# Kernel tuning notes

Hardware: AMD Instinct MI355X
Metric: run time of the kernel (lower is better)

The kernel has to match this reference:

```python
import jax, jax.numpy as jnp
import numpy as np

TAPS = 5
DELAY = 3
ITERATIONS = 2
EPS = 1e-10


def _wpe_one_iteration(Y, power):
    # Y: (B, F, C, T) complex64, power: (B, F, T) float32
    B, F, C, T = Y.shape
    inv_p = 1.0 / jnp.clip(power, EPS)
    Tq = T - DELAY - TAPS + 1  # number of valid frames
    # signal_framing(Y, TAPS, 1)[..., :Tq, :] then reverse last dim:
    # Y_tilde[..., t, k] = Y[..., t + TAPS - 1 - k]  -> (B, F, C, Tq, TAPS)
    Y_tilde = jnp.stack(
        [Y[..., TAPS - 1 - k: TAPS - 1 - k + Tq] for k in range(TAPS)], axis=-1)
    Y_tilde_ip = Y_tilde * inv_p[..., None, DELAY + TAPS - 1:, None]
    # correlation matrix (B, F, taps*C, taps*C)
    R = jnp.einsum('bfdtk,bfetl->bfkdle', jnp.conj(Y_tilde_ip), Y_tilde)
    R = R.reshape(B, F, TAPS * C, TAPS * C)
    # correlation vector (B, F, taps, C, C): indices (k, e, d)
    P = jnp.einsum('bfdtk,bfet->bfked', jnp.conj(Y_tilde_ip),
                   Y[..., DELAY + TAPS - 1:])
    # regularize and invert (batched small complex systems)
    R = R + EPS * jnp.eye(TAPS * C, dtype=R.dtype)
    inv_R = jnp.linalg.inv(R)
    # (B,F,k,e,d) -> (B,F,e,k,d) -> (B,F,C,taps*C)
    vec = jnp.transpose(P, (0, 1, 3, 2, 4)).reshape(B, F, C, TAPS * C)
    # stacked = vec @ inv_R^T  -> (B, F, C, taps*C)
    stacked = jnp.einsum('bfck,bflk->bfcl', vec, inv_R)
    # (B,F,C1,taps,C2) -> filter_matrix_conj (B,F,taps,C2,C1)
    G_conj = jnp.transpose(stacked.reshape(B, F, C, TAPS, C), (0, 1, 3, 4, 2))
    # delayed copies of Y: Y_shift[..., p, :, t] = Y[..., t - DELAY - p] (zero-padded)
    Y_shift = jnp.stack(
        [jnp.pad(Y[..., :T - DELAY - p], [(0, 0)] * 3 + [(DELAY + p, 0)])
         for p in range(TAPS)], axis=-3)  # (B, F, taps, C, T)
    reverb_tail = jnp.einsum('bfpde,bfpdt->bfet', G_conj, Y_shift)
    return Y - reverb_tail


def setup_inputs() -> dict:
    key = jax.random.key(0)
    k1, k2, k3 = jax.random.split(key, 3)
    B, T, C, F = 8, 600, 8, 257
    data_real = jax.random.normal(k1, (B, T, C, F), dtype=jnp.float32)
    data_imag = jax.random.normal(k2, (B, T, C, F), dtype=jnp.float32)
    ilens = jax.random.randint(k3, (B,), 300, T + 1)
    return {"data_real": data_real, "data_imag": data_imag, "ilens": ilens}


def reference(data_real, data_imag, ilens):
    # data: (B, T, C, F) -> (B, F, C, T)
    Y = jax.lax.complex(data_real, data_imag)
    Y = jnp.transpose(Y, (0, 3, 2, 1))
    B, F, C, T = Y.shape
    # use_dnn_mask=False: power averaged over channels -> (B, F, T)
    power = (Y.real ** 2 + Y.imag ** 2).mean(axis=-2)
    enhanced = Y
    for i in range(ITERATIONS):
        if i > 0:
            power = (enhanced.real ** 2 + enhanced.imag ** 2).mean(axis=-2)
        enhanced = _wpe_one_iteration(Y, power)
    # zero out padded frames (make_pad_mask along T)
    tmask = (jnp.arange(T) < ilens[:, None]).astype(enhanced.real.dtype)
    enhanced = enhanced * tmask[:, None, None, :]
    # back to (B, T, C, F)
    enhanced = jnp.transpose(enhanced, (0, 3, 2, 1))
    return enhanced.real, enhanced.imag
```

## Files before the change

### kernel.cpp

```cpp
#include <hip/hip_runtime.h>
#include <hip/hip_bf16.h>

#define Bb 8
#define Tt 600
#define Cc 8
#define Ff 257
#define TAPS 5
#define DELAY 3
#define KC 40
#define NC 48
#define RPW 52
#define TQ 593
#define TP 602
#define EPSF 1e-10f
#define NTOT (Bb*Tt*Cc*Ff)

__device__ __forceinline__ float2 cmul2(float2 a, float2 b) {
  return make_float2(a.x*b.x - a.y*b.y, a.x*b.y + a.y*b.x);
}

#define CMAC(acc, ax, ay, b)                    \
  acc.x = fmaf(ax, b.x, acc.x);                 \
  acc.x = fmaf(ay, b.y, acc.x);                 \
  acc.y = fmaf(ax, b.y, acc.y);                 \
  acc.y = fmaf(-(ay), b.x, acc.y);

__global__ __launch_bounds__(256) void k_tin(const float* __restrict__ in_re,
                                             const float* __restrict__ in_im,
                                             float2* __restrict__ Yt) {
  __shared__ float2 tile[32][33];
  int f0 = blockIdx.x * 32, t0 = blockIdx.y * 32;
  int b = blockIdx.z >> 3, c = blockIdx.z & 7;
  int tx = threadIdx.x & 31, ty = threadIdx.x >> 5;
#pragma unroll
  for (int ii = 0; ii < 4; ++ii) {
    int t = t0 + ty + 8 * ii, f = f0 + tx;
    if (t < Tt && f < Ff) {
      size_t idx = (((size_t)b * Tt + t) * Cc + c) * Ff + f;
      tile[ty + 8 * ii][tx] = make_float2(in_re[idx], in_im[idx]);
    }
  }
  __syncthreads();
#pragma unroll
  for (int ii = 0; ii < 4; ++ii) {
    int f = f0 + ty + 8 * ii, t = t0 + tx;
    if (f < Ff && t < Tt) {
      size_t o = (((size_t)b * Ff + f) * Cc + c) * Tt + t;
      Yt[o] = tile[tx][ty + 8 * ii];
    }
  }
}

#define ABODY(u) do {                                                     \
  float2 ynd = Yd[tb + (u) + 4];                                          \
  float2 yne = Ye[tb + (u) + 4];                                          \
  float2 yep = Ye[tb + (u) + 7];                                          \
  float w = wl[tb + (u) + 7];                                             \
  wd[((u)+4)%5] = ynd; we[((u)+4)%5] = yne;                               \
  float ax[5], ay[5];                                                     \
  _Pragma("unroll")                                                       \
  for (int k = 0; k < 5; ++k) {                                           \
    float2 yr = wd[((u)+4-k)%5]; ax[k] = w*yr.x; ay[k] = w*yr.y;          \
  }                                                                       \
  _Pragma("unroll")                                                       \
  for (int l = 0; l < 5; ++l) {                                           \
    float2 yc = we[((u)+4-l)%5];                                          \
    _Pragma("unroll")                                                     \
    for (int k = 0; k < 5; ++k) { CMAC(rac[k][l], ax[k], ay[k], yc); }    \
  }                                                                       \
  _Pragma("unroll")                                                       \
  for (int k = 0; k < 5; ++k) { CMAC(pac[k], ax[k], ay[k], yep); }        \
} while (0)

__global__ __launch_bounds__(512, 4) void k_wpe(const float2* __restrict__ Yt,
                                                float2* __restrict__ enh,
                                                const float* __restrict__ in_re,
                                                const float* __restrict__ in_im,
                                                const int* __restrict__ ilens,
                                                float* __restrict__ out_re,
                                                float* __restrict__ out_im,
                                                int load_direct, int store_direct) {
  __shared__ float2 Yl[Cc][TP];
  __shared__ float2 RP[KC][RPW];
  __shared__ float wl[Tt];

  int bf = blockIdx.x;
  int b = bf / Ff, f = bf % Ff;
  int tid = threadIdx.x;
  int group = tid >> 6;
  int lane = tid & 63;
  int d = lane & 7;
  int e = lane >> 3;

  if (!load_direct) {
    const float4* Yg = (const float4*)(Yt + (size_t)bf * (Cc * Tt));
    for (int i = tid; i < Cc * Tt / 2; i += 512) {
      float4 v = Yg[i];
      int c = i / (Tt / 2), t2 = (i % (Tt / 2)) * 2;
      *(float4*)&Yl[c][t2] = v;
    }
  } else {
    for (int i = tid; i < Cc * Tt; i += 512) {
      int c = i / Tt, t = i % Tt;
      size_t idx = (((size_t)b * Tt + t) * Cc + c) * Ff + f;
      Yl[c][t] = make_float2(in_re[idx], in_im[idx]);
    }
  }
  __syncthreads();

  const float2* Yd = &Yl[d][0];
  const float2* Ye = &Yl[e][0];

  int tA = (TQ * group) >> 3;
  int tB = (TQ * (group + 1)) >> 3;

  for (int iter = 0; iter < 3; ++iter) {
    if (iter == 0) {
      for (int t = tid; t < Tt; t += 512) {
        float s = 0.f;
#pragma unroll
        for (int c = 0; c < Cc; ++c) { float2 y = Yl[c][t]; s += y.x*y.x + y.y*y.y; }
        wl[t] = 1.0f / fmaxf(s * 0.125f, EPSF);
      }
    } else {
      for (int t = tid; t < Tt; t += 512) {
        float2 acc[Cc];
#pragma unroll
        for (int ee = 0; ee < Cc; ++ee) acc[ee] = Yl[ee][t];
        for (int p = 0; p < TAPS; ++p) {
          int ts = t - DELAY - p;
          if (ts < 0) break;
#pragma unroll
          for (int dd = 0; dd < Cc; ++dd) {
            float2 u = Yl[dd][ts];
            int j = p * Cc + dd;
#pragma unroll
            for (int ee = 0; ee < Cc; ++ee) {
              float2 g = RP[j][KC + ee];
              acc[ee].x -= g.x*u.x - g.y*u.y;
              acc[ee].y -= g.x*u.y + g.y*u.x;
            }
          }
        }
        if (iter == 1) {
          float s = 0.f;
#pragma unroll
          for (int ee = 0; ee < Cc; ++ee) s += acc[ee].x*acc[ee].x + acc[ee].y*acc[ee].y;
          wl[t] = 1.0f / fmaxf(s * 0.125f, EPSF);
        } else {
          if (!store_direct) {
            float2* Eg = enh + (size_t)bf * (Cc * Tt);
#pragma unroll
            for (int ee = 0; ee < Cc; ++ee) Eg[ee * Tt + t] = acc[ee];
          } else {
            int il = ilens[b];
            bool live = (t < il);
#pragma unroll
            for (int ee = 0; ee < Cc; ++ee) {
              float2 v = live ? acc[ee] : make_float2(0.f, 0.f);
              size_t idx = (((size_t)b * Tt + t) * Cc + ee) * Ff + f;
              out_re[idx] = v.x;
              out_im[idx] = v.y;
            }
          }
        }
      }
    }
    if (iter == 2) break;
    __syncthreads();

    float2 rac[5][5], pac[5];
#pragma unroll
    for (int k = 0; k < 5; ++k) {
#pragma unroll
      for (int l = 0; l < 5; ++l) rac[k][l] = make_float2(0.f, 0.f);
      pac[k] = make_float2(0.f, 0.f);
    }

    float2 wd[5], we[5];
#pragma unroll
    for (int i = 0; i < 4; ++i) { wd[i] = Yd[tA + i]; we[i] = Ye[tA + i]; }

    int tb = tA;
    for (; tb + 5 <= tB; tb += 5) {
      ABODY(0); ABODY(1); ABODY(2); ABODY(3); ABODY(4);
    }
    for (int t = tb; t < tB; ++t) {
      float2 yep = Ye[t + 7];
      float w = wl[t + 7];
      float ax[5], ay[5];
#pragma unroll
      for (int k = 0; k < 5; ++k) {
        float2 yr = Yd[t + 4 - k]; ax[k] = w*yr.x; ay[k] = w*yr.y;
      }
#pragma unroll
      for (int l = 0; l < 5; ++l) {
        float2 yc = Ye[t + 4 - l];
#pragma unroll
        for (int k = 0; k < 5; ++k) { CMAC(rac[k][l], ax[k], ay[k], yc); }
      }
#pragma unroll
      for (int k = 0; k < 5; ++k) { CMAC(pac[k], ax[k], ay[k], yep); }
    }

    for (int gpass = 0; gpass < 8; ++gpass) {
      if (group == gpass) {
        if (gpass == 0) {
#pragma unroll
          for (int k = 0; k < 5; ++k) {
#pragma unroll
            for (int l = 0; l < 5; ++l) RP[k*8+d][l*8+e] = rac[k][l];
            RP[k*8+d][KC+e] = pac[k];
          }
        } else {
#pragma unroll
          for (int k = 0; k < 5; ++k) {
#pragma unroll
            for (int l = 0; l < 5; ++l) {
              float2 v = RP[k*8+d][l*8+e];
              v.x += rac[k][l].x; v.y += rac[k][l].y;
              RP[k*8+d][l*8+e] = v;
            }
            float2 v = RP[k*8+d][KC+e];
            v.x += pac[k].x; v.y += pac[k].y;
            RP[k*8+d][KC+e] = v;
          }
        }
      }
      __syncthreads();
    }

    if (tid < KC) RP[tid][tid].x += EPSF;
    __syncthreads();

    for (int j = 0; j < KC; ++j) {
      float2 pv = RP[j][j];
      float idn = 1.0f / (pv.x*pv.x + pv.y*pv.y);
      float2 ip = make_float2(pv.x * idn, -pv.y * idn);
      for (int k = j + 1 + tid; k < NC; k += 512)
        RP[j][k] = cmul2(RP[j][k], ip);
      __syncthreads();
      int ncols = NC - 1 - j;
      int tot = (KC - 1) * ncols;
      for (int idx = tid; idx < tot; idx += 512) {
        int i = idx / ncols;
        if (i >= j) ++i;
        int k = j + 1 + idx % ncols;
        float2 lij = RP[i][j];
        float2 s = cmul2(lij, RP[j][k]);
        RP[i][k].x -= s.x;
        RP[i][k].y -= s.y;
      }
      __syncthreads();
    }
  }
}

__global__ __launch_bounds__(256) void k_tout(const float2* __restrict__ enh,
                                              const int* __restrict__ ilens,
                                              float* __restrict__ out_re,
                                              float* __restrict__ out_im) {
  __shared__ float2 tile[32][33];
  int t0 = blockIdx.x * 32, f0 = blockIdx.y * 32;
  int b = blockIdx.z >> 3, c = blockIdx.z & 7;
  int tx = threadIdx.x & 31, ty = threadIdx.x >> 5;
#pragma unroll
  for (int ii = 0; ii < 4; ++ii) {
    int f = f0 + ty + 8 * ii, t = t0 + tx;
    if (f < Ff && t < Tt)
      tile[ty + 8 * ii][tx] = enh[(((size_t)b * Ff + f) * Cc + c) * Tt + t];
  }
  __syncthreads();
  int il = ilens[b];
#pragma unroll
  for (int ii = 0; ii < 4; ++ii) {
    int t = t0 + ty + 8 * ii, f = f0 + tx;
    if (t < Tt && f < Ff) {
      float2 v = tile[tx][ty + 8 * ii];
      if (t >= il) v = make_float2(0.f, 0.f);
      size_t idx = (((size_t)b * Tt + t) * Cc + c) * Ff + f;
      out_re[idx] = v.x;
      out_im[idx] = v.y;
    }
  }
}

extern "C" void kernel_launch(void* const* d_in, const int* in_sizes, int n_in,
                              void* d_out, int out_size, void* d_ws, size_t ws_size,
                              hipStream_t stream) {
  const float* in_re = (const float*)d_in[0];
  const float* in_im = (const float*)d_in[1];
  const int* ilens = (const int*)d_in[2];
  float* out_re = (float*)d_out;
  float* out_im = out_re + NTOT;

  size_t ybytes = (size_t)Bb * Ff * Cc * Tt * sizeof(float2);
  int have_yt  = ws_size >= ybytes;
  int have_enh = ws_size >= 2 * ybytes;
  float2* Yt  = (float2*)d_ws;
  float2* enh = (float2*)((char*)d_ws + ybytes);

  if (have_yt) {
    dim3 g((Ff + 31) / 32, (Tt + 31) / 32, Bb * Cc);
    k_tin<<<g, dim3(256), 0, stream>>>(in_re, in_im, Yt);
  }
  {
    dim3 g(Bb * Ff);
    k_wpe<<<g, dim3(512), 0, stream>>>(Yt, enh, in_re, in_im, ilens,
                                       out_re, out_im,
                                       have_yt ? 0 : 1, have_enh ? 0 : 1);
  }
  if (have_enh) {
    dim3 g((Tt + 31) / 32, (Ff + 31) / 32, Bb * Cc);
    k_tout<<<g, dim3(256), 0, stream>>>(enh, ilens, out_re, out_im);
  }
}
```

Baseline: 1.203 ms.

## Use shared atomics for R reduction and single-barrier Gauss-Jordan elimination

Replaces the eight serialized per-group passes that accumulated the correlation matrix into shared memory with shared-memory atomicAdds after a zero fill. The elimination now uses one barrier per pivot instead of two: each row scales its multiplier by the pivot's reciprocal on the fly, and the solution columns are normalized once at the end. Eight threads are assigned per row for the update. The aim is to cut barrier count and serialization, at the cost of atomic contention on shared memory and a less balanced mapping of threads to rows.

```diff
diff --git a/kernel.cpp b/kernel.cpp
--- a/kernel.cpp
+++ b/kernel.cpp
@@ -72,14 +72,15 @@
   for (int k = 0; k < 5; ++k) { CMAC(pac[k], ax[k], ay[k], yep); }        \
 } while (0)
 
-__global__ __launch_bounds__(512, 4) void k_wpe(const float2* __restrict__ Yt,
-                                                float2* __restrict__ enh,
-                                                const float* __restrict__ in_re,
-                                                const float* __restrict__ in_im,
-                                                const int* __restrict__ ilens,
-                                                float* __restrict__ out_re,
-                                                float* __restrict__ out_im,
-                                                int load_direct, int store_direct) {
+__global__ __attribute__((amdgpu_waves_per_eu(4)))
+__launch_bounds__(512) void k_wpe(const float2* __restrict__ Yt,
+                                  float2* __restrict__ enh,
+                                  const float* __restrict__ in_re,
+                                  const float* __restrict__ in_im,
+                                  const int* __restrict__ ilens,
+                                  float* __restrict__ out_re,
+                                  float* __restrict__ out_im,
+                                  int load_direct, int store_direct) {
   __shared__ float2 Yl[Cc][TP];
   __shared__ float2 RP[KC][RPW];
   __shared__ float wl[Tt];
@@ -113,6 +114,8 @@
 
   int tA = (TQ * group) >> 3;
   int tB = (TQ * (group + 1)) >> 3;
+  int si = tid >> 3;
+  int sk = tid & 7;
 
   for (int iter = 0; iter < 3; ++iter) {
     if (iter == 0) {
@@ -169,6 +172,12 @@
     if (iter == 2) break;
     __syncthreads();
 
+    {
+      float2* RPf = &RP[0][0];
+      for (int i = tid; i < KC * RPW; i += 512) RPf[i] = make_float2(0.f, 0.f);
+    }
+    __syncthreads();
+
     float2 rac[5][5], pac[5];
 #pragma unroll
     for (int k = 0; k < 5; ++k) {
@@ -203,56 +212,41 @@
       for (int k = 0; k < 5; ++k) { CMAC(pac[k], ax[k], ay[k], yep); }
     }
 
-    for (int gpass = 0; gpass < 8; ++gpass) {
-      if (group == gpass) {
-        if (gpass == 0) {
-#pragma unroll
-          for (int k = 0; k < 5; ++k) {
-#pragma unroll
-            for (int l = 0; l < 5; ++l) RP[k*8+d][l*8+e] = rac[k][l];
-            RP[k*8+d][KC+e] = pac[k];
-          }
-        } else {
-#pragma unroll
-          for (int k = 0; k < 5; ++k) {
-#pragma unroll
-            for (int l = 0; l < 5; ++l) {
-              float2 v = RP[k*8+d][l*8+e];
-              v.x += rac[k][l].x; v.y += rac[k][l].y;
-              RP[k*8+d][l*8+e] = v;
-            }
-            float2 v = RP[k*8+d][KC+e];
-            v.x += pac[k].x; v.y += pac[k].y;
-            RP[k*8+d][KC+e] = v;
-          }
+#pragma unroll
+    for (int k = 0; k < 5; ++k) {
+#pragma unroll
+      for (int l = 0; l < 5; ++l) {
+        atomicAdd(&RP[k * 8 + d][l * 8 + e].x, rac[k][l].x);
+        atomicAdd(&RP[k * 8 + d][l * 8 + e].y, rac[k][l].y);
+      }
+      atomicAdd(&RP[k * 8 + d][KC + e].x, pac[k].x);
+      atomicAdd(&RP[k * 8 + d][KC + e].y, pac[k].y);
+    }
+    if (tid < KC) atomicAdd(&RP[tid][tid].x, EPSF);
+    __syncthreads();
+
+    for (int j = 0; j < KC; ++j) {
+      if (si < KC && si != j) {
+        float2 pv = RP[j][j];
+        float idn = 1.0f / (pv.x * pv.x + pv.y * pv.y);
+        float2 ip = make_float2(pv.x * idn, -pv.y * idn);
+        float2 lij = cmul2(RP[si][j], ip);
+        for (int k = j + 1 + sk; k < NC; k += 8) {
+          float2 s = cmul2(lij, RP[j][k]);
+          RP[si][k].x -= s.x;
+          RP[si][k].y -= s.y;
         }
       }
       __syncthreads();
     }
-
-    if (tid < KC) RP[tid][tid].x += EPSF;
+    if (tid < KC * Cc) {
+      int j = tid >> 3, ee = tid & 7;
+      float2 pv = RP[j][j];
+      float idn = 1.0f / (pv.x * pv.x + pv.y * pv.y);
+      float2 ip = make_float2(pv.x * idn, -pv.y * idn);
+      RP[j][KC + ee] = cmul2(RP[j][KC + ee], ip);
+    }
     __syncthreads();
-
-    for (int j = 0; j < KC; ++j) {
-      float2 pv = RP[j][j];
-      float idn = 1.0f / (pv.x*pv.x + pv.y*pv.y);
-      float2 ip = make_float2(pv.x * idn, -pv.y * idn);
-      for (int k = j + 1 + tid; k < NC; k += 512)
-        RP[j][k] = cmul2(RP[j][k], ip);
-      __syncthreads();
-      int ncols = NC - 1 - j;
-      int tot = (KC - 1) * ncols;
-      for (int idx = tid; idx < tot; idx += 512) {
-        int i = idx / ncols;
-        if (i >= j) ++i;
-        int k = j + 1 + idx % ncols;
-        float2 lij = RP[i][j];
-        float2 s = cmul2(lij, RP[j][k]);
-        RP[i][k].x -= s.x;
-        RP[i][k].y -= s.y;
-      }
-      __syncthreads();
-    }
   }
 }
 
```

Measured after the change: 1.562 ms. 29.8% more time.
